# Optimization experiments

Hardware: AMD Instinct MI355X
Metric: run time of the kernel (lower is better)

Reference implementation:

```python
import jax, jax.numpy as jnp
import numpy as np

B, H, W, C = 32, 256, 256, 3
KH, KW, F = 5, 5, 8


def setup_inputs() -> dict:
    key = jax.random.key(0)
    k1, k2 = jax.random.split(key)
    x = jax.random.normal(k1, (B, H, W, C), dtype=jnp.float32)
    # learned structuring elements, shape (KH, KW, C, F) per build()
    kernel = jax.random.normal(k2, (KH, KW, C, F), dtype=jnp.float32) * 0.1
    return {"x": x, "kernel": kernel}


def _max_of_erosions(x, kernel):
    # tf.nn.erosion2d semantics: out[b,y,x,c] = min_{dy,dx} in[b, y+dy-pt, x+dx-pl, c]
    #                                               - kernel[KH-1-dy, KW-1-dx, c]
    # (erosion = -dilation(-x, reversed kernel)); then channel-max per filter.
    Bq, Hq, Wq, Cq = x.shape
    kh, kw, _, nf = kernel.shape
    pad_h, pad_w = kh - 1, kw - 1          # stride 1, rate 1, SAME padding
    pt, pl = pad_h // 2, pad_w // 2
    xp = jnp.pad(x, ((0, 0), (pt, pad_h - pt), (pl, pad_w - pl), (0, 0)),
                 constant_values=jnp.inf)   # +inf is identity for min
    kflip = kernel[::-1, ::-1]              # reflected structuring element
    ero = None                              # running min over window taps
    for dy in range(kh):                    # small fixed 5x5 tap loop
        for dx in range(kw):
            win = xp[:, dy:dy + Hq, dx:dx + Wq, :]          # [B,H,W,C]
            cand = win[..., None] - kflip[dy, dx]           # [B,H,W,C,F]
            ero = cand if ero is None else jnp.minimum(ero, cand)
    return jnp.max(ero, axis=3)             # channel max -> [B,H,W,F]


def reference(x, kernel):
    return _max_of_erosions(x, kernel)
```

## Files before the change

kernel.cpp:

```cpp
#include <hip/hip_runtime.h>
#include <math.h>


typedef _Float16 h2 __attribute__((ext_vector_type(2)));

static __device__ __forceinline__ h2 cvt_pk(float a, float b) {
    return __builtin_bit_cast(h2, __builtin_amdgcn_cvt_pkrtz(a, b));
}
static __device__ __forceinline__ h2 u2h(unsigned u) {
    return __builtin_bit_cast(h2, u);
}

#define Bq 32
#define Hq 256
#define Wq 256

#define RSTR 792
#define TILE_H2 (8 * RSTR)

#define INF2 0x7C007C00u

__global__ __launch_bounds__(256) void maxero_lds(
    const float* __restrict__ x,
    const float* __restrict__ kern,
    float* __restrict__ out)
{
    __shared__ h2 xlds[TILE_H2];
    __shared__ h2 klds[25 * 12];

    const int tid = threadIdx.x;
    const int bI  = blockIdx.x;
    const int b   = bI >> 6;
    const int h0  = (bI & 63) << 2;

    for (int i = tid; i < 300; i += 256) {
        int tap = i / 12;
        int rem = i - tap * 12;
        int c = rem >> 2, fp = rem & 3;
        int dy = tap / 5, dx = tap - dy * 5;
        const float* kp = kern + (((4 - dy) * 5 + (4 - dx)) * 24) + c * 8 + fp * 2;
        klds[i] = cvt_pk(kp[0], kp[1]);
    }

    const float* xb = x + (size_t)b * (Hq * Wq * 3);
    #pragma unroll
    for (int k = 0; k < 6; ++k) {
        int chunk = tid + k * 256;
        int rr    = chunk / 192;
        int off   = (chunk - rr * 192) * 4;
        int r     = h0 - 2 + rr;
        bool rv   = (unsigned)r < (unsigned)Hq;
        int rc    = min(max(r, 0), Hq - 1);
        const float4 v = *reinterpret_cast<const float4*>(xb + rc * 768 + off);
        h2* d = &xlds[rr * RSTR + 18 + off];
        d[0] = rv ? cvt_pk(v.x, v.x) : u2h(INF2);
        d[1] = rv ? cvt_pk(v.y, v.y) : u2h(INF2);
        d[2] = rv ? cvt_pk(v.z, v.z) : u2h(INF2);
        d[3] = rv ? cvt_pk(v.w, v.w) : u2h(INF2);
    }
    if (tid < 192) {
        int rr = tid / 24, p = tid - rr * 24;
        int idx = rr * RSTR + (p < 18 ? p : 768 + p);
        xlds[idx] = u2h(INF2);
    }
    __syncthreads();

    const int hrow = tid >> 6;
    const int w0   = (tid & 63) << 2;

    h2 ero[4][3][4];
    #pragma unroll
    for (int p = 0; p < 4; ++p)
        #pragma unroll
        for (int c = 0; c < 3; ++c)
            #pragma unroll
            for (int fp = 0; fp < 4; ++fp)
                ero[p][c][fp] = u2h(INF2);

    #pragma unroll
    for (int dy = 0; dy < 5; ++dy) {
        const uint4* rp = reinterpret_cast<const uint4*>(
            &xlds[(hrow + dy) * RSTR + 12 + 3 * w0]);
        uint4 q0 = rp[0], q1 = rp[1], q2 = rp[2], q3 = rp[3], q4 = rp[4], q5 = rp[5];
        const unsigned qf[24] = { q0.x,q0.y,q0.z,q0.w, q1.x,q1.y,q1.z,q1.w,
                                  q2.x,q2.y,q2.z,q2.w, q3.x,q3.y,q3.z,q3.w,
                                  q4.x,q4.y,q4.z,q4.w, q5.x,q5.y,q5.z,q5.w };
        #pragma unroll
        for (int dx = 0; dx < 5; ++dx) {
            const uint4* kk = reinterpret_cast<const uint4*>(&klds[(dy * 5 + dx) * 12]);
            uint4 k0 = kk[0], k1 = kk[1], k2 = kk[2];
            const unsigned kf[12] = { k0.x,k0.y,k0.z,k0.w,
                                      k1.x,k1.y,k1.z,k1.w,
                                      k2.x,k2.y,k2.z,k2.w };
            #pragma unroll
            for (int p = 0; p < 4; ++p)
                #pragma unroll
                for (int c = 0; c < 3; ++c)
                    #pragma unroll
                    for (int fp = 0; fp < 4; ++fp) {
                        h2 cand = u2h(qf[(p + dx) * 3 + c]) - u2h(kf[c * 4 + fp]);
                        ero[p][c][fp] = __builtin_elementwise_min(ero[p][c][fp], cand);
                    }
        }
    }

    #pragma unroll
    for (int p = 0; p < 4; ++p) {
        float of[8];
        #pragma unroll
        for (int fp = 0; fp < 4; ++fp) {
            h2 m = __builtin_elementwise_max(
                       __builtin_elementwise_max(ero[p][0][fp], ero[p][1][fp]),
                       ero[p][2][fp]);
            of[fp * 2 + 0] = (float)m[0];
            of[fp * 2 + 1] = (float)m[1];
        }
        size_t opix = ((size_t)b * 65536 + (size_t)(h0 + hrow) * 256 + (w0 + p));
        float* op = out + opix * 8;
        reinterpret_cast<float4*>(op)[0] = make_float4(of[0], of[1], of[2], of[3]);
        reinterpret_cast<float4*>(op)[1] = make_float4(of[4], of[5], of[6], of[7]);
    }
}

extern "C" void kernel_launch(void* const* d_in, const int* in_sizes, int n_in,
                              void* d_out, int out_size, void* d_ws, size_t ws_size,
                              hipStream_t stream) {
    const float* x    = (const float*)d_in[0];
    const float* kern = (const float*)d_in[1];
    float* out        = (float*)d_out;
    maxero_lds<<<2048, 256, 0, stream>>>(x, kern, out);
}
```

Baseline: 55.69 us.

## Compute 8 pixels per thread over 8-row tiles with fewer blocks

Each block now covers 8 output rows instead of 4, so it loads 12 halo rows into LDS instead of 8 and uses half as many blocks. Each thread computes 8 adjacent pixels instead of 4, which reuses more of its loaded row data across the horizontal taps and cuts halo overhead per output. The dy loop is no longer unrolled, which keeps code size and register pressure in check given the doubled accumulator array (96 packed halves). The trade-off is higher VGPR use, possibly lower occupancy, and half as many blocks to spread across the CUs.

Result: slower. 64.62 us (+16.0%).

```diff
diff --git a/kernel.cpp b/kernel.cpp
--- a/kernel.cpp
+++ b/kernel.cpp
@@ -11,16 +11,13 @@
     return __builtin_bit_cast(h2, u);
 }
 
-#define Bq 32
 #define Hq 256
-#define Wq 256
-
 #define RSTR 792
-#define TILE_H2 (8 * RSTR)
-
+#define TROWS 12
+#define TILE_H2 (TROWS * RSTR)
 #define INF2 0x7C007C00u
 
-__global__ __launch_bounds__(256) void maxero_lds(
+__global__ __launch_bounds__(256) void maxero8(
     const float* __restrict__ x,
     const float* __restrict__ kern,
     float* __restrict__ out)
@@ -30,8 +27,8 @@
 
     const int tid = threadIdx.x;
     const int bI  = blockIdx.x;
-    const int b   = bI >> 6;
-    const int h0  = (bI & 63) << 2;
+    const int b   = bI >> 5;
+    const int h0  = (bI & 31) << 3;
 
     for (int i = tid; i < 300; i += 256) {
         int tap = i / 12;
@@ -42,9 +39,9 @@
         klds[i] = cvt_pk(kp[0], kp[1]);
     }
 
-    const float* xb = x + (size_t)b * (Hq * Wq * 3);
+    const float* xb = x + (size_t)b * (Hq * 256 * 3);
     #pragma unroll
-    for (int k = 0; k < 6; ++k) {
+    for (int k = 0; k < 9; ++k) {
         int chunk = tid + k * 256;
         int rr    = chunk / 192;
         int off   = (chunk - rr * 192) * 4;
@@ -58,54 +55,57 @@
         d[2] = rv ? cvt_pk(v.z, v.z) : u2h(INF2);
         d[3] = rv ? cvt_pk(v.w, v.w) : u2h(INF2);
     }
-    if (tid < 192) {
-        int rr = tid / 24, p = tid - rr * 24;
-        int idx = rr * RSTR + (p < 18 ? p : 768 + p);
-        xlds[idx] = u2h(INF2);
+    for (int i = tid; i < 288; i += 256) {
+        int rr = i / 24, p = i - rr * 24;
+        xlds[rr * RSTR + (p < 18 ? p : 768 + p)] = u2h(INF2);
     }
     __syncthreads();
 
-    const int hrow = tid >> 6;
-    const int w0   = (tid & 63) << 2;
+    const int hrow = tid >> 5;
+    const int w0   = (tid & 31) << 3;
 
-    h2 ero[4][3][4];
+    h2 ero[8][3][4];
     #pragma unroll
-    for (int p = 0; p < 4; ++p)
+    for (int p = 0; p < 8; ++p)
         #pragma unroll
         for (int c = 0; c < 3; ++c)
             #pragma unroll
             for (int fp = 0; fp < 4; ++fp)
                 ero[p][c][fp] = u2h(INF2);
 
-    #pragma unroll
+    #pragma unroll 1
     for (int dy = 0; dy < 5; ++dy) {
         const uint4* rp = reinterpret_cast<const uint4*>(
             &xlds[(hrow + dy) * RSTR + 12 + 3 * w0]);
-        uint4 q0 = rp[0], q1 = rp[1], q2 = rp[2], q3 = rp[3], q4 = rp[4], q5 = rp[5];
-        const unsigned qf[24] = { q0.x,q0.y,q0.z,q0.w, q1.x,q1.y,q1.z,q1.w,
-                                  q2.x,q2.y,q2.z,q2.w, q3.x,q3.y,q3.z,q3.w,
-                                  q4.x,q4.y,q4.z,q4.w, q5.x,q5.y,q5.z,q5.w };
+        unsigned xq[36];
+        #pragma unroll
+        for (int q = 0; q < 9; ++q) {
+            uint4 t = rp[q];
+            xq[q * 4 + 0] = t.x; xq[q * 4 + 1] = t.y;
+            xq[q * 4 + 2] = t.z; xq[q * 4 + 3] = t.w;
+        }
+        const uint4* kb = reinterpret_cast<const uint4*>(&klds[dy * 60]);
         #pragma unroll
         for (int dx = 0; dx < 5; ++dx) {
-            const uint4* kk = reinterpret_cast<const uint4*>(&klds[(dy * 5 + dx) * 12]);
-            uint4 k0 = kk[0], k1 = kk[1], k2 = kk[2];
-            const unsigned kf[12] = { k0.x,k0.y,k0.z,k0.w,
-                                      k1.x,k1.y,k1.z,k1.w,
-                                      k2.x,k2.y,k2.z,k2.w };
+            uint4 k0 = kb[dx * 3 + 0], k1 = kb[dx * 3 + 1], k2 = kb[dx * 3 + 2];
+            const unsigned kf[12] = { k0.x, k0.y, k0.z, k0.w,
+                                      k1.x, k1.y, k1.z, k1.w,
+                                      k2.x, k2.y, k2.z, k2.w };
             #pragma unroll
-            for (int p = 0; p < 4; ++p)
+            for (int p = 0; p < 8; ++p)
                 #pragma unroll
                 for (int c = 0; c < 3; ++c)
                     #pragma unroll
                     for (int fp = 0; fp < 4; ++fp) {
-                        h2 cand = u2h(qf[(p + dx) * 3 + c]) - u2h(kf[c * 4 + fp]);
+                        h2 cand = u2h(xq[(p + dx) * 3 + c]) - u2h(kf[c * 4 + fp]);
                         ero[p][c][fp] = __builtin_elementwise_min(ero[p][c][fp], cand);
                     }
         }
     }
 
+    const size_t rowbase = (size_t)b * 65536 + (size_t)(h0 + hrow) * 256 + w0;
     #pragma unroll
-    for (int p = 0; p < 4; ++p) {
+    for (int p = 0; p < 8; ++p) {
         float of[8];
         #pragma unroll
         for (int fp = 0; fp < 4; ++fp) {
@@ -115,8 +115,7 @@
             of[fp * 2 + 0] = (float)m[0];
             of[fp * 2 + 1] = (float)m[1];
         }
-        size_t opix = ((size_t)b * 65536 + (size_t)(h0 + hrow) * 256 + (w0 + p));
-        float* op = out + opix * 8;
+        float* op = out + (rowbase + p) * 8;
         reinterpret_cast<float4*>(op)[0] = make_float4(of[0], of[1], of[2], of[3]);
         reinterpret_cast<float4*>(op)[1] = make_float4(of[4], of[5], of[6], of[7]);
     }
@@ -128,5 +127,5 @@
     const float* x    = (const float*)d_in[0];
     const float* kern = (const float*)d_in[1];
     float* out        = (float*)d_out;
-    maxero_lds<<<2048, 256, 0, stream>>>(x, kern, out);
+    maxero8<<<1024, 256, 0, stream>>>(x, kern, out);
 }
```

## Switch erosion kernel from packed fp16 to fp32 with filter-half loop

Applied to the files above, without the earlier changes.

Replaces the packed half-precision min/sub computation with full fp32 arithmetic and stores the input tile in LDS as fp32. Filters are processed in two halves of four to limit register pressure. Kernel weights are read directly from global memory, which the compiler can place in scalar loads, instead of being staged in LDS. This restores fp32 accuracy but gives up the two-wide packed math, so ALU work roughly doubles.

Result: slower. 65.73 us (+18.0%).

```diff
diff --git a/kernel.cpp b/kernel.cpp
--- a/kernel.cpp
+++ b/kernel.cpp
@@ -2,47 +2,23 @@
 #include <math.h>
 
 
-typedef _Float16 h2 __attribute__((ext_vector_type(2)));
+#define Hq 256
 
-static __device__ __forceinline__ h2 cvt_pk(float a, float b) {
-    return __builtin_bit_cast(h2, __builtin_amdgcn_cvt_pkrtz(a, b));
-}
-static __device__ __forceinline__ h2 u2h(unsigned u) {
-    return __builtin_bit_cast(h2, u);
-}
-
-#define Bq 32
-#define Hq 256
-#define Wq 256
-
-#define RSTR 792
-#define TILE_H2 (8 * RSTR)
-
-#define INF2 0x7C007C00u
-
-__global__ __launch_bounds__(256) void maxero_lds(
+__global__ __launch_bounds__(256) void maxero_f32(
     const float* __restrict__ x,
     const float* __restrict__ kern,
     float* __restrict__ out)
 {
-    __shared__ h2 xlds[TILE_H2];
-    __shared__ h2 klds[25 * 12];
+    __shared__ __align__(16) float xt[8 * 792];
 
     const int tid = threadIdx.x;
     const int bI  = blockIdx.x;
     const int b   = bI >> 6;
     const int h0  = (bI & 63) << 2;
 
-    for (int i = tid; i < 300; i += 256) {
-        int tap = i / 12;
-        int rem = i - tap * 12;
-        int c = rem >> 2, fp = rem & 3;
-        int dy = tap / 5, dx = tap - dy * 5;
-        const float* kp = kern + (((4 - dy) * 5 + (4 - dx)) * 24) + c * 8 + fp * 2;
-        klds[i] = cvt_pk(kp[0], kp[1]);
-    }
+    const float INF = __builtin_inff();
 
-    const float* xb = x + (size_t)b * (Hq * Wq * 3);
+    const float* xb = x + (size_t)b * (Hq * 256 * 3);
     #pragma unroll
     for (int k = 0; k < 6; ++k) {
         int chunk = tid + k * 256;
@@ -51,74 +27,78 @@
         int r     = h0 - 2 + rr;
         bool rv   = (unsigned)r < (unsigned)Hq;
         int rc    = min(max(r, 0), Hq - 1);
-        const float4 v = *reinterpret_cast<const float4*>(xb + rc * 768 + off);
-        h2* d = &xlds[rr * RSTR + 18 + off];
-        d[0] = rv ? cvt_pk(v.x, v.x) : u2h(INF2);
-        d[1] = rv ? cvt_pk(v.y, v.y) : u2h(INF2);
-        d[2] = rv ? cvt_pk(v.z, v.z) : u2h(INF2);
-        d[3] = rv ? cvt_pk(v.w, v.w) : u2h(INF2);
+        float4 v = *reinterpret_cast<const float4*>(xb + rc * 768 + off);
+        float2* d = reinterpret_cast<float2*>(&xt[rr * 792 + 18 + off]);
+        d[0] = rv ? make_float2(v.x, v.y) : make_float2(INF, INF);
+        d[1] = rv ? make_float2(v.z, v.w) : make_float2(INF, INF);
     }
     if (tid < 192) {
         int rr = tid / 24, p = tid - rr * 24;
-        int idx = rr * RSTR + (p < 18 ? p : 768 + p);
-        xlds[idx] = u2h(INF2);
+        xt[rr * 792 + (p < 18 ? p : 768 + p)] = INF;
     }
     __syncthreads();
 
     const int hrow = tid >> 6;
     const int w0   = (tid & 63) << 2;
+    const size_t rowbase = (size_t)b * 65536 + (size_t)(h0 + hrow) * 256 + w0;
 
-    h2 ero[4][3][4];
-    #pragma unroll
-    for (int p = 0; p < 4; ++p)
+    #pragma unroll 1
+    for (int fh = 0; fh < 2; ++fh) {
+        const float* kub = kern + fh * 4;
+
+        float acc[4][3][4];
         #pragma unroll
-        for (int c = 0; c < 3; ++c)
+        for (int p = 0; p < 4; ++p)
             #pragma unroll
-            for (int fp = 0; fp < 4; ++fp)
-                ero[p][c][fp] = u2h(INF2);
+            for (int c = 0; c < 3; ++c)
+                #pragma unroll
+                for (int j = 0; j < 4; ++j)
+                    acc[p][c][j] = INF;
 
-    #pragma unroll
-    for (int dy = 0; dy < 5; ++dy) {
-        const uint4* rp = reinterpret_cast<const uint4*>(
-            &xlds[(hrow + dy) * RSTR + 12 + 3 * w0]);
-        uint4 q0 = rp[0], q1 = rp[1], q2 = rp[2], q3 = rp[3], q4 = rp[4], q5 = rp[5];
-        const unsigned qf[24] = { q0.x,q0.y,q0.z,q0.w, q1.x,q1.y,q1.z,q1.w,
-                                  q2.x,q2.y,q2.z,q2.w, q3.x,q3.y,q3.z,q3.w,
-                                  q4.x,q4.y,q4.z,q4.w, q5.x,q5.y,q5.z,q5.w };
         #pragma unroll
-        for (int dx = 0; dx < 5; ++dx) {
-            const uint4* kk = reinterpret_cast<const uint4*>(&klds[(dy * 5 + dx) * 12]);
-            uint4 k0 = kk[0], k1 = kk[1], k2 = kk[2];
-            const unsigned kf[12] = { k0.x,k0.y,k0.z,k0.w,
-                                      k1.x,k1.y,k1.z,k1.w,
-                                      k2.x,k2.y,k2.z,k2.w };
+        for (int dy = 0; dy < 5; ++dy) {
+            const float4* rp = reinterpret_cast<const float4*>(
+                &xt[(hrow + dy) * 792 + 12 + 3 * w0]);
+            float xr[24];
             #pragma unroll
-            for (int p = 0; p < 4; ++p)
+            for (int q = 0; q < 6; ++q) {
+                float4 t = rp[q];
+                xr[q * 4 + 0] = t.x; xr[q * 4 + 1] = t.y;
+                xr[q * 4 + 2] = t.z; xr[q * 4 + 3] = t.w;
+            }
+            #pragma unroll
+            for (int c = 0; c < 3; ++c)
                 #pragma unroll
-                for (int c = 0; c < 3; ++c)
+                for (int j = 0; j < 4; ++j) {
+                    float k0 = kub[((4 - dy) * 5 + 4) * 24 + c * 8 + j];
+                    float k1 = kub[((4 - dy) * 5 + 3) * 24 + c * 8 + j];
+                    float k2 = kub[((4 - dy) * 5 + 2) * 24 + c * 8 + j];
+                    float k3 = kub[((4 - dy) * 5 + 1) * 24 + c * 8 + j];
+                    float k4 = kub[((4 - dy) * 5 + 0) * 24 + c * 8 + j];
                     #pragma unroll
-                    for (int fp = 0; fp < 4; ++fp) {
-                        h2 cand = u2h(qf[(p + dx) * 3 + c]) - u2h(kf[c * 4 + fp]);
-                        ero[p][c][fp] = __builtin_elementwise_min(ero[p][c][fp], cand);
+                    for (int p = 0; p < 4; ++p) {
+                        float c0 = xr[(p + 0) * 3 + c] - k0;
+                        float c1 = xr[(p + 1) * 3 + c] - k1;
+                        float c2 = xr[(p + 2) * 3 + c] - k2;
+                        float c3 = xr[(p + 3) * 3 + c] - k3;
+                        float c4 = xr[(p + 4) * 3 + c] - k4;
+                        float a = acc[p][c][j];
+                        a = fminf(fminf(a, c0), c1);
+                        a = fminf(fminf(a, c2), c3);
+                        acc[p][c][j] = fminf(a, c4);
                     }
+                }
         }
-    }
 
-    #pragma unroll
-    for (int p = 0; p < 4; ++p) {
-        float of[8];
         #pragma unroll
-        for (int fp = 0; fp < 4; ++fp) {
-            h2 m = __builtin_elementwise_max(
-                       __builtin_elementwise_max(ero[p][0][fp], ero[p][1][fp]),
-                       ero[p][2][fp]);
-            of[fp * 2 + 0] = (float)m[0];
-            of[fp * 2 + 1] = (float)m[1];
+        for (int p = 0; p < 4; ++p) {
+            float4 o;
+            o.x = fmaxf(fmaxf(acc[p][0][0], acc[p][1][0]), acc[p][2][0]);
+            o.y = fmaxf(fmaxf(acc[p][0][1], acc[p][1][1]), acc[p][2][1]);
+            o.z = fmaxf(fmaxf(acc[p][0][2], acc[p][1][2]), acc[p][2][2]);
+            o.w = fmaxf(fmaxf(acc[p][0][3], acc[p][1][3]), acc[p][2][3]);
+            *reinterpret_cast<float4*>(out + (rowbase + p) * 8 + fh * 4) = o;
         }
-        size_t opix = ((size_t)b * 65536 + (size_t)(h0 + hrow) * 256 + (w0 + p));
-        float* op = out + opix * 8;
-        reinterpret_cast<float4*>(op)[0] = make_float4(of[0], of[1], of[2], of[3]);
-        reinterpret_cast<float4*>(op)[1] = make_float4(of[4], of[5], of[6], of[7]);
     }
 }
 
@@ -128,5 +108,5 @@
     const float* x    = (const float*)d_in[0];
     const float* kern = (const float*)d_in[1];
     float* out        = (float*)d_out;
-    maxero_lds<<<2048, 256, 0, stream>>>(x, kern, out);
+    maxero_f32<<<2048, 256, 0, stream>>>(x, kern, out);
 }
```
